# Kernel tuning notes

Measured on AMD Instinct MI355X. Metric: run time of the kernel, lower is better.

## Reference

```python
import jax, jax.numpy as jnp
import numpy as np

N = 100000
E = 1600000
H, C = 4, 64
NEG_SLOPE = 0.2


def setup_inputs() -> dict:
    key = jax.random.key(0)
    ks = jax.random.split(key, 12)
    def rn(k, shape, scale=1.0):
        return jax.random.normal(k, shape, dtype=jnp.float32) * scale
    return {
        "x": rn(ks[0], (N, 3)),
        "edge_index": jax.random.randint(ks[1], (2, E), 0, N, dtype=jnp.int64),
        "W1": rn(ks[2], (3, H * C), 0.5),
        "a_src1": rn(ks[3], (H, C), 0.1),
        "a_dst1": rn(ks[4], (H, C), 0.1),
        "b1": jnp.zeros((H * C,), jnp.float32),
        "W2": rn(ks[5], (H * C, H * C), 0.06),
        "a_src2": rn(ks[6], (H, C), 0.1),
        "a_dst2": rn(ks[7], (H, C), 0.1),
        "b2": jnp.zeros((H * C,), jnp.float32),
        "fc_w": rn(ks[8], (H * C, 2), 0.06),
        "fc_b": jnp.zeros((2,), jnp.float32),
    }


def _gat_layer(x, src, dst, W, a_src, a_dst, bias):
    # x: [N, F_in] -> h: [N, H, C]
    h = (x @ W).reshape(N, H, C)
    # per-node attention logits
    al_src = jnp.einsum("nhc,hc->nh", h, a_src)  # [N, H]
    al_dst = jnp.einsum("nhc,hc->nh", h, a_dst)  # [N, H]
    e = jax.nn.leaky_relu(al_src[src] + al_dst[dst], NEG_SLOPE)  # [E', H]
    # segment softmax over incoming edges of each dst node
    m = jax.ops.segment_max(e, dst, num_segments=N)  # [N, H]
    m = jnp.where(jnp.isfinite(m), m, 0.0)
    ex = jnp.exp(e - m[dst])
    denom = jax.ops.segment_sum(ex, dst, num_segments=N)  # [N, H]
    alpha = ex / (denom[dst] + 1e-16)  # [E', H]
    # scatter-aggregate messages
    out = jax.ops.segment_sum(h[src] * alpha[:, :, None], dst, num_segments=N)
    return out.reshape(N, H * C) + bias


def reference(x, edge_index, W1, a_src1, a_dst1, b1, W2, a_src2, a_dst2, b2, fc_w, fc_b):
    # add self-loops (PyG GATConv default)
    loop = jnp.arange(N, dtype=edge_index.dtype)
    src = jnp.concatenate([edge_index[0], loop])
    dst = jnp.concatenate([edge_index[1], loop])
    h = _gat_layer(x, src, dst, W1, a_src1, a_dst1, b1)
    h = jax.nn.relu(h)
    h = _gat_layer(h, src, dst, W2, a_src2, a_dst2, b2)
    h = jax.nn.relu(h)
    return h @ fc_w + fc_b
```

## Files before the change

kernel.cpp:

```cpp
#include <hip/hip_runtime.h>

#define NN 100000
#define NE 1600000
#define HC 256
#define NB_SCAN 98

typedef __attribute__((ext_vector_type(8))) short short8;
typedef __attribute__((ext_vector_type(4))) float f32x4;

__device__ __forceinline__ float4 ld4(const float* p) { return *(const float4*)p; }
__device__ __forceinline__ unsigned short f2bf(float f) {
    unsigned u = __float_as_uint(f);
    return (unsigned short)((u + 0x7fffu + ((u >> 16) & 1u)) >> 16);
}
__device__ __forceinline__ float bf2f(unsigned short h) { return __uint_as_float(((unsigned)h) << 16); }

__device__ __forceinline__ void unpack8(uint4 v, float* f) {
    f[0] = __uint_as_float(v.x << 16); f[1] = __uint_as_float(v.x & 0xffff0000u);
    f[2] = __uint_as_float(v.y << 16); f[3] = __uint_as_float(v.y & 0xffff0000u);
    f[4] = __uint_as_float(v.z << 16); f[5] = __uint_as_float(v.z & 0xffff0000u);
    f[6] = __uint_as_float(v.w << 16); f[7] = __uint_as_float(v.w & 0xffff0000u);
}

__global__ void k_count_rank(const int* __restrict__ dst, int* __restrict__ counts,
                             int* __restrict__ rank) {
    int i = blockIdx.x * blockDim.x + threadIdx.x;
    if (i < NE) rank[i] = atomicAdd(&counts[dst[i]], 1);
}

__global__ void k_scan1(const int* __restrict__ counts, int* __restrict__ offs,
                        int* __restrict__ partials) {
    __shared__ int sh[1024];
    int b = blockIdx.x, t = threadIdx.x, i = b * 1024 + t;
    int v = (i < NN) ? counts[i] : 0;
    sh[t] = v;
    __syncthreads();
    for (int o = 1; o < 1024; o <<= 1) {
        int y = (t >= o) ? sh[t - o] : 0;
        __syncthreads();
        sh[t] += y;
        __syncthreads();
    }
    if (i < NN) offs[i] = sh[t] - v;
    if (t == 1023) partials[b] = sh[t];
}

__global__ void k_scan2(const int* __restrict__ partials, int* __restrict__ carries) {
    __shared__ int sh[128];
    int t = threadIdx.x;
    int v = (t < NB_SCAN) ? partials[t] : 0;
    sh[t] = v;
    __syncthreads();
    for (int o = 1; o < 128; o <<= 1) {
        int y = (t >= o) ? sh[t - o] : 0;
        __syncthreads();
        sh[t] += y;
        __syncthreads();
    }
    if (t < NB_SCAN) carries[t] = sh[t] - v;
}

__global__ void k_scan3(const int* __restrict__ carries, int* __restrict__ offs) {
    int b = blockIdx.x, i = b * 1024 + threadIdx.x;
    if (i < NN) offs[i] += carries[b];
    if (i == 0) offs[NN] = NE;
}

__global__ void k_place(const int* __restrict__ src, const int* __restrict__ dst,
                        const int* __restrict__ rank, const int* __restrict__ offs,
                        int* __restrict__ csr) {
    int i = blockIdx.x * blockDim.x + threadIdx.x;
    if (i < NE) csr[offs[dst[i]] + rank[i]] = src[i];
}

__global__ void k_prep_p1(const float* __restrict__ W1, const float* __restrict__ as1,
                          const float* __restrict__ ad1, float* __restrict__ ps1,
                          float* __restrict__ pd1) {
    int t = threadIdx.x;
    int h = t >> 6, cc = t & 63;
    float avs = as1[h * 64 + cc], avd = ad1[h * 64 + cc];
    for (int k = 0; k < 3; ++k) {
        float w = W1[k * 256 + h * 64 + cc];
        float vs = w * avs, vd = w * avd;
        #pragma unroll
        for (int m = 1; m < 64; m <<= 1) { vs += __shfl_xor(vs, m, 64); vd += __shfl_xor(vd, m, 64); }
        if (cc == 0) { ps1[h * 4 + k] = vs; pd1[h * 4 + k] = vd; }
    }
}

__global__ void k_prep_bt(const float* __restrict__ W2, unsigned short* __restrict__ Bt) {
    int vk = blockIdx.x, c = threadIdx.x;
    float v = W2[(size_t)(vk & 255) * HC + c];
    unsigned short hi = f2bf(v);
    unsigned short o = (vk < 256) ? hi : f2bf(v - bf2f(hi));
    Bt[(size_t)c * 512 + vk] = o;
}

__global__ __launch_bounds__(256) void k_agg1(
    const float* __restrict__ x, const float* __restrict__ W1,
    const float* __restrict__ ps1, const float* __restrict__ pd1,
    const int* __restrict__ offs, const int* __restrict__ csr,
    const float* __restrict__ b1, unsigned short* __restrict__ zh) {
    __shared__ float Y[16][16];
    int t = threadIdx.x;
    int g = t >> 4, l16 = t & 15;
    int d = blockIdx.x * 16 + g;
    float ps[4][3], pd[4][3];
    #pragma unroll
    for (int h = 0; h < 4; ++h) {
        ps[h][0] = ps1[h * 4 + 0]; ps[h][1] = ps1[h * 4 + 1]; ps[h][2] = ps1[h * 4 + 2];
        pd[h][0] = pd1[h * 4 + 0]; pd[h][1] = pd1[h * 4 + 1]; pd[h][2] = pd1[h * 4 + 2];
    }
    float xd0 = x[d * 3], xd1 = x[d * 3 + 1], xd2 = x[d * 3 + 2];
    float ald[4];
    #pragma unroll
    for (int h = 0; h < 4; ++h) ald[h] = xd0 * pd[h][0] + xd1 * pd[h][1] + xd2 * pd[h][2];
    float S[4] = {0.f, 0.f, 0.f, 0.f};
    float X0[4] = {0.f, 0.f, 0.f, 0.f}, X1[4] = {0.f, 0.f, 0.f, 0.f}, X2[4] = {0.f, 0.f, 0.f, 0.f};
    int beg = offs[d], end = offs[d + 1];
    for (int idx = beg + l16; idx < end; idx += 16) {
        int sn = csr[idx] * 3;
        float a0 = x[sn], a1 = x[sn + 1], a2 = x[sn + 2];
        #pragma unroll
        for (int h = 0; h < 4; ++h) {
            float e = a0 * ps[h][0] + a1 * ps[h][1] + a2 * ps[h][2] + ald[h];
            e = e > 0.f ? e : 0.2f * e;
            float p = __expf(e);
            S[h] += p; X0[h] += p * a0; X1[h] += p * a1; X2[h] += p * a2;
        }
    }
    if (l16 == 0) {
        #pragma unroll
        for (int h = 0; h < 4; ++h) {
            float e = xd0 * ps[h][0] + xd1 * ps[h][1] + xd2 * ps[h][2] + ald[h];
            e = e > 0.f ? e : 0.2f * e;
            float p = __expf(e);
            S[h] += p; X0[h] += p * xd0; X1[h] += p * xd1; X2[h] += p * xd2;
        }
    }
    #pragma unroll
    for (int m = 1; m < 16; m <<= 1) {
        #pragma unroll
        for (int h = 0; h < 4; ++h) {
            S[h] += __shfl_xor(S[h], m, 64);
            X0[h] += __shfl_xor(X0[h], m, 64);
            X1[h] += __shfl_xor(X1[h], m, 64);
            X2[h] += __shfl_xor(X2[h], m, 64);
        }
    }
    if (l16 == 0) {
        *(float4*)&Y[g][0]  = make_float4(S[0], S[1], S[2], S[3]);
        *(float4*)&Y[g][4]  = make_float4(X0[0], X0[1], X0[2], X0[3]);
        *(float4*)&Y[g][8]  = make_float4(X1[0], X1[1], X1[2], X1[3]);
        *(float4*)&Y[g][12] = make_float4(X2[0], X2[1], X2[2], X2[3]);
    }
    __syncthreads();
    int lane = t & 63, w = t >> 6;
    int head = lane >> 4, c = lane << 2;
    float4 w0 = ld4(W1 + c), w1 = ld4(W1 + 256 + c), w2 = ld4(W1 + 512 + c);
    float4 bv = ld4(b1 + c);
    #pragma unroll
    for (int rr = 0; rr < 4; ++rr) {
        int g2 = w * 4 + rr;
        int d2 = blockIdx.x * 16 + g2;
        float inv = 1.f / Y[g2][head];
        float Y0 = Y[g2][4 + head] * inv;
        float Y1 = Y[g2][8 + head] * inv;
        float Y2 = Y[g2][12 + head] * inv;
        float4 z;
        z.x = fmaxf(Y0 * w0.x + Y1 * w1.x + Y2 * w2.x + bv.x, 0.f);
        z.y = fmaxf(Y0 * w0.y + Y1 * w1.y + Y2 * w2.y + bv.y, 0.f);
        z.z = fmaxf(Y0 * w0.z + Y1 * w1.z + Y2 * w2.z + bv.z, 0.f);
        z.w = fmaxf(Y0 * w0.w + Y1 * w1.w + Y2 * w2.w + bv.w, 0.f);
        ushort4 hi;
        hi.x = f2bf(z.x); hi.y = f2bf(z.y); hi.z = f2bf(z.z); hi.w = f2bf(z.w);
        *(ushort4*)(zh + (size_t)d2 * HC + c) = hi;
    }
}

__global__ __launch_bounds__(512) void k_gemm2_mfma(
    const unsigned short* __restrict__ zh, const unsigned short* __restrict__ Bt,
    const float* __restrict__ a_s, const float* __restrict__ a_d,
    unsigned short* __restrict__ h2bf, float* __restrict__ alS2,
    float* __restrict__ alD2) {
    __shared__ __align__(16) unsigned short As[128 * 64];
    __shared__ __align__(16) unsigned short Bs[256 * 64];
    int t = threadIdx.x;
    int l = t & 63, w = t >> 6;
    int wm = w >> 2, wn = w & 3;
    int lr = l & 15, lk = l >> 4;
    int row0 = blockIdx.x * 128;

    f32x4 acc[4][4];
    f32x4 z4 = {0.f, 0.f, 0.f, 0.f};
    #pragma unroll
    for (int i = 0; i < 4; ++i)
        #pragma unroll
        for (int j = 0; j < 4; ++j) acc[i][j] = z4;

    int sa_row = t >> 2, sa_q = t & 3;
    const unsigned short* zrow = zh + (size_t)(row0 + sa_row) * HC;
    bool a_ok = (row0 + sa_row) < NN;
    int sb_col = t >> 1, sb_h = t & 1;
    const unsigned short* btrow = Bt + (size_t)sb_col * 512;

    for (int kt = 0; kt < 8; ++kt) {
        int ksb = kt * 64;
        int acol0 = ksb & 255;
        uint4 av0 = make_uint4(0, 0, 0, 0), av1 = make_uint4(0, 0, 0, 0);
        if (a_ok) {
            av0 = *(const uint4*)(zrow + acol0 + sa_q * 16);
            av1 = *(const uint4*)(zrow + acol0 + sa_q * 16 + 8);
        }
        int rs = sa_row * 64;
        *(uint4*)&As[rs + ((2 * sa_q) ^ (sa_row & 7)) * 8] = av0;
        *(uint4*)&As[rs + ((2 * sa_q + 1) ^ (sa_row & 7)) * 8] = av1;
        const unsigned short* bsrc = btrow + ksb + sb_h * 32;
        int cs = sb_col * 64;
        #pragma unroll
        for (int j = 0; j < 4; ++j) {
            uint4 bv = *(const uint4*)(bsrc + j * 8);
            *(uint4*)&Bs[cs + ((sb_h * 4 + j) ^ (sb_col & 7)) * 8] = bv;
        }
        __syncthreads();
        #pragma unroll
        for (int s = 0; s < 2; ++s) {
            short8 af[4], bfr[4];
            #pragma unroll
            for (int fi = 0; fi < 4; ++fi) {
                int row = wm * 64 + fi * 16 + lr;
                int kg = (s * 4 + lk) ^ (row & 7);
                af[fi] = *(const short8*)&As[row * 64 + kg * 8];
            }
            #pragma unroll
            for (int bj = 0; bj < 4; ++bj) {
                int col = wn * 64 + bj * 16 + lr;
                int kg = (s * 4 + lk) ^ (col & 7);
                bfr[bj] = *(const short8*)&Bs[col * 64 + kg * 8];
            }
            #pragma unroll
            for (int fi = 0; fi < 4; ++fi)
                #pragma unroll
                for (int bj = 0; bj < 4; ++bj)
                    acc[fi][bj] = __builtin_amdgcn_mfma_f32_16x16x32_bf16(af[fi], bfr[bj], acc[fi][bj], 0, 0, 0);
        }
        __syncthreads();
    }

    float asr[4], adr[4];
    #pragma unroll
    for (int bj = 0; bj < 4; ++bj) {
        int cc = wn * 64 + bj * 16 + lr;
        asr[bj] = a_s[cc];
        adr[bj] = a_d[cc];
    }
    #pragma unroll
    for (int fi = 0; fi < 4; ++fi) {
        #pragma unroll
        for (int r = 0; r < 4; ++r) {
            int grow = row0 + wm * 64 + fi * 16 + lk * 4 + r;
            bool ok = grow < NN;
            float ps = 0.f, pd = 0.f;
            #pragma unroll
            for (int bj = 0; bj < 4; ++bj) {
                float vv = acc[fi][bj][r];
                if (ok) h2bf[(size_t)grow * HC + wn * 64 + bj * 16 + lr] = f2bf(vv);
                ps += vv * asr[bj];
                pd += vv * adr[bj];
            }
            #pragma unroll
            for (int mm = 1; mm < 16; mm <<= 1) {
                ps += __shfl_xor(ps, mm, 64);
                pd += __shfl_xor(pd, mm, 64);
            }
            if (ok && lr == 0) {
                alS2[grow * 4 + wn] = ps;
                alD2[grow * 4 + wn] = pd;
            }
        }
    }
}

__global__ __launch_bounds__(256) void k_prep_p(
    const float* __restrict__ alS2, const float* __restrict__ alD2,
    const int* __restrict__ offs, const int* __restrict__ csr,
    float* __restrict__ pw) {
    int gt = blockIdx.x * blockDim.x + threadIdx.x;
    int d = gt >> 4;
    int l16 = threadIdx.x & 15;
    int head = l16 & 3;
    int eo = l16 >> 2;
    float ad = alD2[d * 4 + head];
    int beg = offs[d], end = offs[d + 1];
    for (int idx = beg + eo; idx < end; idx += 4) {
        int sn = csr[idx];
        float e = alS2[sn * 4 + head] + ad;
        e = e > 0.f ? e : 0.2f * e;
        pw[(size_t)idx * 4 + head] = __expf(e);
    }
}

__global__ __launch_bounds__(256) void k_agg2(
    const unsigned short* __restrict__ h2bf, const float* __restrict__ alS2,
    const float* __restrict__ alD2, const int* __restrict__ offs,
    const int* __restrict__ csr, const float* __restrict__ pw,
    const float* __restrict__ b2, const float* __restrict__ fcw,
    const float* __restrict__ fcb, float* __restrict__ out) {
    int gt = blockIdx.x * blockDim.x + threadIdx.x;
    int d = gt >> 4;
    int l16 = threadIdx.x & 15;
    int head = l16 >> 2;
    int cb = l16 * 16;
    float e0 = alS2[d * 4 + head] + alD2[d * 4 + head];
    e0 = e0 > 0.f ? e0 : 0.2f * e0;
    float s = __expf(e0);
    float acc[16], f[16];
    {
        const uint4* rp = (const uint4*)(h2bf + (size_t)d * HC + cb);
        uint4 r0 = rp[0], r1 = rp[1];
        unpack8(r0, f); unpack8(r1, f + 8);
        #pragma unroll
        for (int j = 0; j < 16; ++j) acc[j] = s * f[j];
    }
    int beg = offs[d], end = offs[d + 1];
    if (beg < end) {
        int i1 = (beg + 1 < end) ? beg + 1 : beg;
        int sn0 = csr[beg];
        float pv0 = pw[(size_t)beg * 4 + head];
        const uint4* rp0 = (const uint4*)(h2bf + (size_t)sn0 * HC + cb);
        uint4 a0 = rp0[0], b0 = rp0[1];
        int sn1 = csr[i1];
        float pv1 = (beg + 1 < end) ? pw[(size_t)(beg + 1) * 4 + head] : 0.f;
        const uint4* rp1 = (const uint4*)(h2bf + (size_t)sn1 * HC + cb);
        uint4 a1 = rp1[0], b1v = rp1[1];
        for (int i = beg; i < end; ++i) {
            int nx = i + 2;
            bool okn = nx < end;
            int snn = okn ? csr[nx] : sn0;
            float pvn = okn ? pw[(size_t)nx * 4 + head] : 0.f;
            const uint4* rpn = (const uint4*)(h2bf + (size_t)snn * HC + cb);
            uint4 an = rpn[0], bn = rpn[1];
            unpack8(a0, f); unpack8(b0, f + 8);
            s += pv0;
            #pragma unroll
            for (int j = 0; j < 16; ++j) acc[j] += pv0 * f[j];
            a0 = a1; b0 = b1v; pv0 = pv1;
            a1 = an; b1v = bn; pv1 = pvn;
        }
    }
    float inv = 1.f / (s + 1e-16f);
    float p0 = 0.f, p1 = 0.f;
    #pragma unroll
    for (int q = 0; q < 4; ++q) {
        float4 bv = ld4(b2 + cb + q * 4);
        float4 fa = ld4(fcw + (cb + q * 4) * 2);
        float4 fb = ld4(fcw + (cb + q * 4) * 2 + 4);
        float o0 = fmaxf(acc[q * 4 + 0] * inv + bv.x, 0.f);
        float o1 = fmaxf(acc[q * 4 + 1] * inv + bv.y, 0.f);
        float o2 = fmaxf(acc[q * 4 + 2] * inv + bv.z, 0.f);
        float o3 = fmaxf(acc[q * 4 + 3] * inv + bv.w, 0.f);
        p0 += o0 * fa.x + o1 * fa.z + o2 * fb.x + o3 * fb.z;
        p1 += o0 * fa.y + o1 * fa.w + o2 * fb.y + o3 * fb.w;
    }
    #pragma unroll
    for (int mm = 1; mm < 16; mm <<= 1) {
        p0 += __shfl_xor(p0, mm, 64);
        p1 += __shfl_xor(p1, mm, 64);
    }
    if (l16 == 0) {
        out[d * 2 + 0] = p0 + fcb[0];
        out[d * 2 + 1] = p1 + fcb[1];
    }
}

extern "C" void kernel_launch(void* const* d_in, const int* in_sizes, int n_in,
                              void* d_out, int out_size, void* d_ws, size_t ws_size,
                              hipStream_t stream) {
    const float* x   = (const float*)d_in[0];
    const int*   ei  = (const int*)d_in[1];
    const float* W1  = (const float*)d_in[2];
    const float* as1 = (const float*)d_in[3];
    const float* ad1 = (const float*)d_in[4];
    const float* b1  = (const float*)d_in[5];
    const float* W2  = (const float*)d_in[6];
    const float* as2 = (const float*)d_in[7];
    const float* ad2 = (const float*)d_in[8];
    const float* b2  = (const float*)d_in[9];
    const float* fcw = (const float*)d_in[10];
    const float* fcb = (const float*)d_in[11];
    float* out = (float*)d_out;

    char* p = (char*)d_ws;
    unsigned short* zh   = (unsigned short*)p; p += (size_t)NN * HC * 2;
    unsigned short* h2bf = (unsigned short*)p; p += (size_t)NN * HC * 2;
    float* alS2 = (float*)p; p += (size_t)NN * 4 * 4;
    float* alD2 = (float*)p; p += (size_t)NN * 4 * 4;
    float* ps1  = (float*)p; p += 256;
    float* pd1  = (float*)p; p += 256;
    int* counts = (int*)p;   p += (size_t)NN * 4;
    int* offs   = (int*)p;   p += (size_t)(NN + 2) * 4;
    int* rank   = (int*)p;   p += (size_t)NE * 4;
    int* csr    = (int*)p;   p += (size_t)NE * 4;
    float* pw   = (float*)p; p += (size_t)NE * 4 * 4;
    int* partials = (int*)p; p += 512;
    int* carries  = (int*)p; p += 512;
    unsigned short* Bt = (unsigned short*)counts;

    const int* e_src = ei;
    const int* e_dst = ei + NE;

    hipMemsetAsync(counts, 0, NN * sizeof(int), stream);
    k_count_rank<<<(NE + 255) / 256, 256, 0, stream>>>(e_dst, counts, rank);
    k_scan1<<<NB_SCAN, 1024, 0, stream>>>(counts, offs, partials);
    k_scan2<<<1, 128, 0, stream>>>(partials, carries);
    k_scan3<<<NB_SCAN, 1024, 0, stream>>>(carries, offs);
    k_place<<<(NE + 255) / 256, 256, 0, stream>>>(e_src, e_dst, rank, offs, csr);

    k_prep_bt<<<512, 256, 0, stream>>>(W2, Bt);
    k_prep_p1<<<1, 256, 0, stream>>>(W1, as1, ad1, ps1, pd1);

    k_agg1<<<NN / 16, 256, 0, stream>>>(x, W1, ps1, pd1, offs, csr, b1, zh);
    k_gemm2_mfma<<<(NN + 127) / 128, 512, 0, stream>>>(zh, Bt, as2, ad2, h2bf, alS2, alD2);
    k_prep_p<<<NN / 16, 256, 0, stream>>>(alS2, alD2, offs, csr, pw);
    k_agg2<<<NN / 16, 256, 0, stream>>>(h2bf, alS2, alD2, offs, csr, pw, b2,
                                        fcw, fcb, out);
}
```

Before: 333.2 us.

## Build CSR via two-level bucket sort instead of per-node atomic counting

Replaces the global per-destination atomic count, three-kernel scan and placement with a coarse two-pass scheme. Edges are histogrammed into 196 buckets of 512 destinations using shared-memory atomics, scattered into bucket order, and then each bucket is sorted locally in LDS to produce offsets and the CSR array. This is meant to cut contention on 100k global atomics and the number of scan launches. In exchange it adds an extra 8-byte-per-edge intermediate buffer, and the order of edges within a destination becomes nondeterministic.

```diff
diff --git a/kernel.cpp b/kernel.cpp
--- a/kernel.cpp
+++ b/kernel.cpp
@@ -3,7 +3,7 @@
 #define NN 100000
 #define NE 1600000
 #define HC 256
-#define NB_SCAN 98
+#define NBUCK 196
 
 typedef __attribute__((ext_vector_type(8))) short short8;
 typedef __attribute__((ext_vector_type(4))) float f32x4;
@@ -22,55 +22,80 @@
     f[6] = __uint_as_float(v.w << 16); f[7] = __uint_as_float(v.w & 0xffff0000u);
 }
 
-__global__ void k_count_rank(const int* __restrict__ dst, int* __restrict__ counts,
-                             int* __restrict__ rank) {
+__global__ __launch_bounds__(256) void k_bhist(const int* __restrict__ dst,
+                                               int* __restrict__ bhist) {
+    __shared__ int h[NBUCK];
+    int t = threadIdx.x;
+    for (int j = t; j < NBUCK; j += 256) h[j] = 0;
+    __syncthreads();
+    int base = blockIdx.x * 2048;
+    int lim = min(base + 2048, NE);
+    for (int i = base + t; i < lim; i += 256)
+        atomicAdd(&h[dst[i] >> 9], 1);
+    __syncthreads();
+    for (int j = t; j < NBUCK; j += 256) if (h[j]) atomicAdd(&bhist[j], h[j]);
+}
+
+__global__ void k_bscan(const int* __restrict__ bhist, int* __restrict__ boffs,
+                        int* __restrict__ bcursor, int* __restrict__ offs) {
+    __shared__ int sh[256];
+    int t = threadIdx.x;
+    int v = (t < NBUCK) ? bhist[t] : 0;
+    sh[t] = v;
+    __syncthreads();
+    for (int o = 1; o < 256; o <<= 1) {
+        int y = (t >= o) ? sh[t - o] : 0;
+        __syncthreads();
+        sh[t] += y;
+        __syncthreads();
+    }
+    if (t < NBUCK) { int e = sh[t] - v; boffs[t] = e; bcursor[t] = e; }
+    if (t == 0) { boffs[NBUCK] = NE; offs[NN] = NE; }
+}
+
+__global__ void k_bscatter(const int* __restrict__ src, const int* __restrict__ dst,
+                           int* __restrict__ bcursor, int2* __restrict__ eb) {
     int i = blockIdx.x * blockDim.x + threadIdx.x;
-    if (i < NE) rank[i] = atomicAdd(&counts[dst[i]], 1);
-}
-
-__global__ void k_scan1(const int* __restrict__ counts, int* __restrict__ offs,
-                        int* __restrict__ partials) {
-    __shared__ int sh[1024];
-    int b = blockIdx.x, t = threadIdx.x, i = b * 1024 + t;
-    int v = (i < NN) ? counts[i] : 0;
-    sh[t] = v;
-    __syncthreads();
-    for (int o = 1; o < 1024; o <<= 1) {
-        int y = (t >= o) ? sh[t - o] : 0;
-        __syncthreads();
-        sh[t] += y;
-        __syncthreads();
-    }
-    if (i < NN) offs[i] = sh[t] - v;
-    if (t == 1023) partials[b] = sh[t];
-}
-
-__global__ void k_scan2(const int* __restrict__ partials, int* __restrict__ carries) {
-    __shared__ int sh[128];
-    int t = threadIdx.x;
-    int v = (t < NB_SCAN) ? partials[t] : 0;
-    sh[t] = v;
-    __syncthreads();
-    for (int o = 1; o < 128; o <<= 1) {
-        int y = (t >= o) ? sh[t - o] : 0;
-        __syncthreads();
-        sh[t] += y;
-        __syncthreads();
-    }
-    if (t < NB_SCAN) carries[t] = sh[t] - v;
-}
-
-__global__ void k_scan3(const int* __restrict__ carries, int* __restrict__ offs) {
-    int b = blockIdx.x, i = b * 1024 + threadIdx.x;
-    if (i < NN) offs[i] += carries[b];
-    if (i == 0) offs[NN] = NE;
-}
-
-__global__ void k_place(const int* __restrict__ src, const int* __restrict__ dst,
-                        const int* __restrict__ rank, const int* __restrict__ offs,
-                        int* __restrict__ csr) {
-    int i = blockIdx.x * blockDim.x + threadIdx.x;
-    if (i < NE) csr[offs[dst[i]] + rank[i]] = src[i];
+    if (i < NE) {
+        int d = dst[i];
+        int p = atomicAdd(&bcursor[d >> 9], 1);
+        eb[p] = make_int2(src[i], d);
+    }
+}
+
+__global__ __launch_bounds__(512) void k_bsort(const int2* __restrict__ eb,
+                                               const int* __restrict__ boffs,
+                                               int* __restrict__ offs,
+                                               int* __restrict__ csr) {
+    __shared__ int hist[512];
+    __shared__ int sc[512];
+    int b = blockIdx.x, t = threadIdx.x;
+    int beg = boffs[b], end = boffs[b + 1];
+    hist[t] = 0;
+    __syncthreads();
+    for (int i = beg + t; i < end; i += 512)
+        atomicAdd(&hist[eb[i].y & 511], 1);
+    __syncthreads();
+    int v = hist[t];
+    sc[t] = v;
+    __syncthreads();
+    for (int o = 1; o < 512; o <<= 1) {
+        int y = (t >= o) ? sc[t - o] : 0;
+        __syncthreads();
+        sc[t] += y;
+        __syncthreads();
+    }
+    int mypos = beg + sc[t] - v;
+    int gd = b * 512 + t;
+    if (gd < NN) offs[gd] = mypos;
+    __syncthreads();
+    hist[t] = mypos;
+    __syncthreads();
+    for (int i = beg + t; i < end; i += 512) {
+        int2 e = eb[i];
+        int p = atomicAdd(&hist[e.y & 511], 1);
+        csr[p] = e.x;
+    }
 }
 
 __global__ void k_prep_p1(const float* __restrict__ W1, const float* __restrict__ as1,
@@ -397,24 +422,23 @@
     float* alD2 = (float*)p; p += (size_t)NN * 4 * 4;
     float* ps1  = (float*)p; p += 256;
     float* pd1  = (float*)p; p += 256;
-    int* counts = (int*)p;   p += (size_t)NN * 4;
+    unsigned short* Bt = (unsigned short*)p; p += (size_t)256 * 512 * 2;
     int* offs   = (int*)p;   p += (size_t)(NN + 2) * 4;
-    int* rank   = (int*)p;   p += (size_t)NE * 4;
     int* csr    = (int*)p;   p += (size_t)NE * 4;
+    int2* eb    = (int2*)p;  p += (size_t)NE * 8;
     float* pw   = (float*)p; p += (size_t)NE * 4 * 4;
-    int* partials = (int*)p; p += 512;
-    int* carries  = (int*)p; p += 512;
-    unsigned short* Bt = (unsigned short*)counts;
+    int* bhist  = (int*)p;   p += 1024;
+    int* boffs  = (int*)p;   p += 1024;
+    int* bcursor= (int*)p;   p += 1024;
 
     const int* e_src = ei;
     const int* e_dst = ei + NE;
 
-    hipMemsetAsync(counts, 0, NN * sizeof(int), stream);
-    k_count_rank<<<(NE + 255) / 256, 256, 0, stream>>>(e_dst, counts, rank);
-    k_scan1<<<NB_SCAN, 1024, 0, stream>>>(counts, offs, partials);
-    k_scan2<<<1, 128, 0, stream>>>(partials, carries);
-    k_scan3<<<NB_SCAN, 1024, 0, stream>>>(carries, offs);
-    k_place<<<(NE + 255) / 256, 256, 0, stream>>>(e_src, e_dst, rank, offs, csr);
+    hipMemsetAsync(bhist, 0, NBUCK * sizeof(int), stream);
+    k_bhist<<<(NE + 2047) / 2048, 256, 0, stream>>>(e_dst, bhist);
+    k_bscan<<<1, 256, 0, stream>>>(bhist, boffs, bcursor, offs);
+    k_bscatter<<<(NE + 255) / 256, 256, 0, stream>>>(e_src, e_dst, bcursor, eb);
+    k_bsort<<<NBUCK, 512, 0, stream>>>(eb, boffs, offs, csr);
 
     k_prep_bt<<<512, 256, 0, stream>>>(W2, Bt);
     k_prep_p1<<<1, 256, 0, stream>>>(W1, as1, ad1, ps1, pd1);
```

Measured after the change: 1.180 ms. 3.54x slower.
